# Optimization experiments

Hardware: AMD Instinct MI355X
Metric: run time of the kernel (lower is better)

## Reference

```python
import jax, jax.numpy as jnp
from jax import lax
import numpy as np

K = 31      # avg_pool2d kernel_size
PAD = 15    # avg_pool2d padding
EPS = 1.0
GAMMA = 5.0


def _box_avg(x):
    # Separable 31x31 box filter, stride 1, zero padding 15,
    # count_include_pad=True (PyTorch default) -> always divide by K*K.
    s = lax.reduce_window(x, 0.0, lax.add, (1, 1, K, 1), (1, 1, 1, 1),
                          [(0, 0), (0, 0), (PAD, PAD), (0, 0)])
    s = lax.reduce_window(s, 0.0, lax.add, (1, 1, 1, K), (1, 1, 1, 1),
                          [(0, 0), (0, 0), (0, 0), (PAD, PAD)])
    return s / (K * K)


def setup_inputs() -> dict:
    key = jax.random.key(0)
    k1, k2 = jax.random.split(key)
    shape = (64, 1, 512, 512)  # [B, C, H, W]
    inp = jax.random.uniform(k1, shape, dtype=jnp.float32)
    tgt = jax.random.uniform(k2, shape, dtype=jnp.float32)
    return {"input": inp, "target": tgt}


def reference(input, target):
    weight = 1.0 + GAMMA * jnp.abs(_box_avg(target) - target)
    intersection = jnp.sum(input * target * weight)
    denom = jnp.sum(input * weight) + jnp.sum(target * weight)
    dice = (2.0 * intersection + EPS) / (denom + EPS)
    return 1.0 - dice
```

## Files before the change

### kernel.cpp

```cpp
#include <hip/hip_runtime.h>
#include <hip/hip_bf16.h>


#define BATCH 64
#define H     512
#define W     512
#define PADR  15
#define RBAND 32
#define RING  38
#define NBLK  (BATCH * (H / RBAND))

static __device__ __forceinline__ unsigned pack2(float e, float o) {
    __hip_bfloat162 h = __float22bfloat162_rn(make_float2(e, o));
    unsigned u; __builtin_memcpy(&u, &h, 4); return u;
}
static __device__ __forceinline__ float2 unpk(unsigned u) {
    return make_float2(__uint_as_float(u << 16),
                       __uint_as_float(u & 0xffff0000u));
}

__global__ __launch_bounds__(256, 4) void fused_kernel(const float* __restrict__ tgt,
                                                       const float* __restrict__ inp,
                                                       float4* __restrict__ partials) {
    const int tid  = threadIdx.x;
    const int lane = tid & 63;
    const int wv   = tid >> 6;
    const int blk  = blockIdx.x;
    const int band = blk & 15;
    const int b    = blk >> 4;
    const int R0   = band * RBAND;
    const float* timg = tgt + (size_t)b * H * W;
    const float* iimg = inp + (size_t)b * H * W;

    __shared__ __align__(16) unsigned ring[RING * 256];

    const int col0 = lane * 8;
    const int ofs  = lane * 4;

    for (int k = 0; k < 10; ++k) {
        const int r_off = wv + 4 * k;
        if (r_off < RING) {
            const int row = R0 - 15 + r_off;
            float4 v0 = make_float4(0.f, 0.f, 0.f, 0.f), v1 = v0;
            if (row >= 0) {
                v0 = *(const float4*)(timg + (size_t)row * W + col0);
                v1 = *(const float4*)(timg + (size_t)row * W + col0 + 4);
            }
            uint4 u;
            u.x = pack2(v0.x, v0.y); u.y = pack2(v0.z, v0.w);
            u.z = pack2(v1.x, v1.y); u.w = pack2(v1.z, v1.w);
            *(uint4*)&ring[((row + RING) % RING) * 256 + ofs] = u;
        }
    }
    __syncthreads();

    const float mL1 = (lane >= 1) ? 1.f : 0.f;
    const float mR1 = (lane <= 62) ? 1.f : 0.f;
    const float mL2 = (lane >= 2) ? 1.f : 0.f;
    const float mR2 = (lane <= 61) ? 1.f : 0.f;

    float vr[8];
    #pragma unroll
    for (int k = 0; k < 8; ++k) vr[k] = 0.f;
    #pragma unroll
    for (int jj = -PADR; jj <= PADR; ++jj) {
        const int rr = R0 + wv + jj;
        const uint4 c = *(const uint4*)&ring[((rr + RING) % RING) * 256 + ofs];
        const float2 e0 = unpk(c.x), e1 = unpk(c.y), e2 = unpk(c.z), e3 = unpk(c.w);
        vr[0] += e0.x; vr[1] += e0.y; vr[2] += e1.x; vr[3] += e1.y;
        vr[4] += e2.x; vr[5] += e2.y; vr[6] += e3.x; vr[7] += e3.y;
    }

    const float inv = 1.0f / 961.0f;
    float aI = 0.f, aA = 0.f, aB = 0.f;

    for (int j = 0; j < 8; ++j) {
        const int h = R0 + 4 * j + wv;

        float4 pf0 = make_float4(0.f, 0.f, 0.f, 0.f), pf1 = pf0;
        const int prow = R0 + 4 * j + 23 + wv;
        if (j < 7 && prow < H) {
            pf0 = *(const float4*)(timg + (size_t)prow * W + col0);
            pf1 = *(const float4*)(timg + (size_t)prow * W + col0 + 4);
        }
        const float4 i0 = *(const float4*)(iimg + (size_t)h * W + col0);
        const float4 i1 = *(const float4*)(iimg + (size_t)h * W + col0 + 4);

        const uint4 tc = *(const uint4*)&ring[(h % RING) * 256 + ofs];

        uint4 ua[4], us[4];
        if (j < 7) {
            #pragma unroll
            for (int q = 0; q < 4; ++q) {
                const int ar = h + 16 + q;
                ua[q] = (ar < H) ? *(const uint4*)&ring[(ar % RING) * 256 + ofs]
                                 : make_uint4(0u, 0u, 0u, 0u);
                us[q] = *(const uint4*)&ring[(((h - 15 + q) + RING) % RING) * 256 + ofs];
            }
        }

        const float p1 = vr[0];
        const float p2 = p1 + vr[1];
        const float p3 = p2 + vr[2];
        const float p4 = p3 + vr[3];
        const float p5 = p4 + vr[4];
        const float p6 = p5 + vr[5];
        const float p7 = p6 + vr[6];
        const float s  = p7 + vr[7];
        const float f1 = s - p1, f2 = s - p2, f3 = s - p3, f4 = s - p4;
        const float f5 = s - p5, f6 = s - p6, f7 = s - p7;

        const float sL1 = __shfl_up(s, 1, 64);
        const float sR1 = __shfl_down(s, 1, 64);
        const float g1 = __shfl_up(f1, 2, 64);
        const float g2 = __shfl_up(f2, 2, 64);
        const float g3 = __shfl_up(f3, 2, 64);
        const float g4 = __shfl_up(f4, 2, 64);
        const float g5 = __shfl_up(f5, 2, 64);
        const float g6 = __shfl_up(f6, 2, 64);
        const float g7 = __shfl_up(f7, 2, 64);
        const float q1 = __shfl_down(p1, 2, 64);
        const float q2 = __shfl_down(p2, 2, 64);
        const float q3 = __shfl_down(p3, 2, 64);
        const float q4 = __shfl_down(p4, 2, 64);
        const float q5 = __shfl_down(p5, 2, 64);
        const float q6 = __shfl_down(p6, 2, 64);
        const float q7 = __shfl_down(p7, 2, 64);

        const float S3 = fmaf(mL1, sL1, fmaf(mR1, sR1, s));
        float win[8];
        win[0] = fmaf(mL2, g1, S3);
        win[1] = fmaf(mL2, g2, fmaf(mR2, q1, S3));
        win[2] = fmaf(mL2, g3, fmaf(mR2, q2, S3));
        win[3] = fmaf(mL2, g4, fmaf(mR2, q3, S3));
        win[4] = fmaf(mL2, g5, fmaf(mR2, q4, S3));
        win[5] = fmaf(mL2, g6, fmaf(mR2, q5, S3));
        win[6] = fmaf(mL2, g7, fmaf(mR2, q6, S3));
        win[7] = fmaf(mR2, q7, S3);

        const float2 t0 = unpk(tc.x), t1 = unpk(tc.y), t2 = unpk(tc.z), t3 = unpk(tc.w);
        const float tv[8] = {t0.x, t0.y, t1.x, t1.y, t2.x, t2.y, t3.x, t3.y};
        const float iv[8] = {i0.x, i0.y, i0.z, i0.w, i1.x, i1.y, i1.z, i1.w};

        #pragma unroll
        for (int k = 0; k < 8; ++k) {
            const float wgt = fmaf(5.0f, fabsf(fmaf(win[k], inv, -tv[k])), 1.0f);
            aI += iv[k] * tv[k] * wgt;
            aA += iv[k] * wgt;
            aB += tv[k] * wgt;
        }

        if (j < 7) {
            #pragma unroll
            for (int q = 0; q < 4; ++q) {
                const float2 a0 = unpk(ua[q].x), a1 = unpk(ua[q].y),
                             a2 = unpk(ua[q].z), a3 = unpk(ua[q].w);
                const float2 s0 = unpk(us[q].x), s1 = unpk(us[q].y),
                             s2 = unpk(us[q].z), s3 = unpk(us[q].w);
                vr[0] += a0.x - s0.x; vr[1] += a0.y - s0.y;
                vr[2] += a1.x - s1.x; vr[3] += a1.y - s1.y;
                vr[4] += a2.x - s2.x; vr[5] += a2.y - s2.y;
                vr[6] += a3.x - s3.x; vr[7] += a3.y - s3.y;
            }
        }
        __syncthreads();

        if (j < 7 && prow < H) {
            uint4 u;
            u.x = pack2(pf0.x, pf0.y); u.y = pack2(pf0.z, pf0.w);
            u.z = pack2(pf1.x, pf1.y); u.w = pack2(pf1.z, pf1.w);
            *(uint4*)&ring[(prow % RING) * 256 + ofs] = u;
        }
        __syncthreads();
    }

    #pragma unroll
    for (int off = 32; off > 0; off >>= 1) {
        aI += __shfl_down(aI, off, 64);
        aA += __shfl_down(aA, off, 64);
        aB += __shfl_down(aB, off, 64);
    }
    float* rf = (float*)ring;
    if (lane == 0) { rf[wv] = aI; rf[8 + wv] = aA; rf[16 + wv] = aB; }
    __syncthreads();
    if (tid == 0) {
        float4 o;
        o.x = rf[0] + rf[1] + rf[2] + rf[3];
        o.y = rf[8] + rf[9] + rf[10] + rf[11];
        o.z = rf[16] + rf[17] + rf[18] + rf[19];
        o.w = 0.f;
        partials[blk] = o;
    }
}

__global__ __launch_bounds__(1024) void reduce_kernel(const float4* __restrict__ partials,
                                                      float* __restrict__ out) {
    const int tid = threadIdx.x;
    const float4 v = partials[tid];
    float aI = v.x, aA = v.y, aB = v.z;
    #pragma unroll
    for (int off = 32; off > 0; off >>= 1) {
        aI += __shfl_down(aI, off, 64);
        aA += __shfl_down(aA, off, 64);
        aB += __shfl_down(aB, off, 64);
    }
    __shared__ float s[3][16];
    const int wvx = tid >> 6, ln = tid & 63;
    if (ln == 0) { s[0][wvx] = aI; s[1][wvx] = aA; s[2][wvx] = aB; }
    __syncthreads();
    if (tid == 0) {
        float I = 0.f, A = 0.f, Bv = 0.f;
        #pragma unroll
        for (int k = 0; k < 16; ++k) { I += s[0][k]; A += s[1][k]; Bv += s[2][k]; }
        out[0] = 1.0f - (2.0f * I + 1.0f) / (A + Bv + 1.0f);
    }
}

extern "C" void kernel_launch(void* const* d_in, const int* in_sizes, int n_in,
                              void* d_out, int out_size, void* d_ws, size_t ws_size,
                              hipStream_t stream) {
    const float* inp = (const float*)d_in[0];
    const float* tgt = (const float*)d_in[1];
    float* out = (float*)d_out;

    float4* partials = (float4*)d_ws;

    fused_kernel<<<NBLK, 256, 0, stream>>>(tgt, inp, partials);
    reduce_kernel<<<1, 1024, 0, stream>>>(partials, out);
}
```

Baseline: 150.8 us.

## Replace shared-memory bf16 ring with per-wave global-load sliding window over 8-row bands

Drops the LDS ring buffer and bf16 packing. Each wave now handles its own 8-row band independently, reading target rows directly from global memory (relying on L2/cache), and the per-iteration __syncthreads barriers go away. The trade-off is more redundant global traffic: each wave re-reads 31 halo rows to seed its vertical sum plus add/subtract rows every step, roughly 4x more target reads per output row. In exchange the computation stays in full fp32 instead of bf16.

```diff
diff --git a/kernel.cpp b/kernel.cpp
--- a/kernel.cpp
+++ b/kernel.cpp
@@ -1,23 +1,13 @@
 #include <hip/hip_runtime.h>
-#include <hip/hip_bf16.h>
 
 
 #define BATCH 64
 #define H     512
 #define W     512
-#define PADR  15
-#define RBAND 32
-#define RING  38
-#define NBLK  (BATCH * (H / RBAND))
-
-static __device__ __forceinline__ unsigned pack2(float e, float o) {
-    __hip_bfloat162 h = __float22bfloat162_rn(make_float2(e, o));
-    unsigned u; __builtin_memcpy(&u, &h, 4); return u;
-}
-static __device__ __forceinline__ float2 unpk(unsigned u) {
-    return make_float2(__uint_as_float(u << 16),
-                       __uint_as_float(u & 0xffff0000u));
-}
+#define RB    8
+#define BANDS (H / RB)
+#define TASKS (BATCH * BANDS)
+#define NBLK  (TASKS / 4)
 
 __global__ __launch_bounds__(256, 4) void fused_kernel(const float* __restrict__ tgt,
                                                        const float* __restrict__ inp,
@@ -25,34 +15,13 @@
     const int tid  = threadIdx.x;
     const int lane = tid & 63;
     const int wv   = tid >> 6;
-    const int blk  = blockIdx.x;
-    const int band = blk & 15;
-    const int b    = blk >> 4;
-    const int R0   = band * RBAND;
+    const int task = blockIdx.x * 4 + wv;
+    const int band = task & (BANDS - 1);
+    const int b    = task >> 6;
+    const int R0   = band * RB;
     const float* timg = tgt + (size_t)b * H * W;
     const float* iimg = inp + (size_t)b * H * W;
-
-    __shared__ __align__(16) unsigned ring[RING * 256];
-
     const int col0 = lane * 8;
-    const int ofs  = lane * 4;
-
-    for (int k = 0; k < 10; ++k) {
-        const int r_off = wv + 4 * k;
-        if (r_off < RING) {
-            const int row = R0 - 15 + r_off;
-            float4 v0 = make_float4(0.f, 0.f, 0.f, 0.f), v1 = v0;
-            if (row >= 0) {
-                v0 = *(const float4*)(timg + (size_t)row * W + col0);
-                v1 = *(const float4*)(timg + (size_t)row * W + col0 + 4);
-            }
-            uint4 u;
-            u.x = pack2(v0.x, v0.y); u.y = pack2(v0.z, v0.w);
-            u.z = pack2(v1.x, v1.y); u.w = pack2(v1.z, v1.w);
-            *(uint4*)&ring[((row + RING) % RING) * 256 + ofs] = u;
-        }
-    }
-    __syncthreads();
 
     const float mL1 = (lane >= 1) ? 1.f : 0.f;
     const float mR1 = (lane <= 62) ? 1.f : 0.f;
@@ -63,40 +32,38 @@
     #pragma unroll
     for (int k = 0; k < 8; ++k) vr[k] = 0.f;
     #pragma unroll
-    for (int jj = -PADR; jj <= PADR; ++jj) {
-        const int rr = R0 + wv + jj;
-        const uint4 c = *(const uint4*)&ring[((rr + RING) % RING) * 256 + ofs];
-        const float2 e0 = unpk(c.x), e1 = unpk(c.y), e2 = unpk(c.z), e3 = unpk(c.w);
-        vr[0] += e0.x; vr[1] += e0.y; vr[2] += e1.x; vr[3] += e1.y;
-        vr[4] += e2.x; vr[5] += e2.y; vr[6] += e3.x; vr[7] += e3.y;
+    for (int jj = -15; jj <= 15; ++jj) {
+        const int r = R0 + jj;
+        if (r >= 0 && r < H) {
+            const float4 a = *(const float4*)(timg + (size_t)r * W + col0);
+            const float4 c = *(const float4*)(timg + (size_t)r * W + col0 + 4);
+            vr[0] += a.x; vr[1] += a.y; vr[2] += a.z; vr[3] += a.w;
+            vr[4] += c.x; vr[5] += c.y; vr[6] += c.z; vr[7] += c.w;
+        }
     }
 
     const float inv = 1.0f / 961.0f;
     float aI = 0.f, aA = 0.f, aB = 0.f;
 
-    for (int j = 0; j < 8; ++j) {
-        const int h = R0 + 4 * j + wv;
+    #pragma unroll 2
+    for (int s = 0; s < RB; ++s) {
+        const int h  = R0 + s;
+        const int ar = h + 16;
+        const int sr = h - 15;
 
-        float4 pf0 = make_float4(0.f, 0.f, 0.f, 0.f), pf1 = pf0;
-        const int prow = R0 + 4 * j + 23 + wv;
-        if (j < 7 && prow < H) {
-            pf0 = *(const float4*)(timg + (size_t)prow * W + col0);
-            pf1 = *(const float4*)(timg + (size_t)prow * W + col0 + 4);
-        }
         const float4 i0 = *(const float4*)(iimg + (size_t)h * W + col0);
         const float4 i1 = *(const float4*)(iimg + (size_t)h * W + col0 + 4);
-
-        const uint4 tc = *(const uint4*)&ring[(h % RING) * 256 + ofs];
-
-        uint4 ua[4], us[4];
-        if (j < 7) {
-            #pragma unroll
-            for (int q = 0; q < 4; ++q) {
-                const int ar = h + 16 + q;
-                ua[q] = (ar < H) ? *(const uint4*)&ring[(ar % RING) * 256 + ofs]
-                                 : make_uint4(0u, 0u, 0u, 0u);
-                us[q] = *(const uint4*)&ring[(((h - 15 + q) + RING) % RING) * 256 + ofs];
-            }
+        const float4 t0 = *(const float4*)(timg + (size_t)h * W + col0);
+        const float4 t1 = *(const float4*)(timg + (size_t)h * W + col0 + 4);
+        float4 a0 = make_float4(0.f, 0.f, 0.f, 0.f), a1 = a0;
+        float4 u0 = a0, u1 = a0;
+        if (ar < H) {
+            a0 = *(const float4*)(timg + (size_t)ar * W + col0);
+            a1 = *(const float4*)(timg + (size_t)ar * W + col0 + 4);
+        }
+        if (sr >= 0) {
+            u0 = *(const float4*)(timg + (size_t)sr * W + col0);
+            u1 = *(const float4*)(timg + (size_t)sr * W + col0 + 4);
         }
 
         const float p1 = vr[0];
@@ -106,12 +73,12 @@
         const float p5 = p4 + vr[4];
         const float p6 = p5 + vr[5];
         const float p7 = p6 + vr[6];
-        const float s  = p7 + vr[7];
-        const float f1 = s - p1, f2 = s - p2, f3 = s - p3, f4 = s - p4;
-        const float f5 = s - p5, f6 = s - p6, f7 = s - p7;
+        const float sS = p7 + vr[7];
+        const float f1 = sS - p1, f2 = sS - p2, f3 = sS - p3, f4 = sS - p4;
+        const float f5 = sS - p5, f6 = sS - p6, f7 = sS - p7;
 
-        const float sL1 = __shfl_up(s, 1, 64);
-        const float sR1 = __shfl_down(s, 1, 64);
+        const float sL1 = __shfl_up(sS, 1, 64);
+        const float sR1 = __shfl_down(sS, 1, 64);
         const float g1 = __shfl_up(f1, 2, 64);
         const float g2 = __shfl_up(f2, 2, 64);
         const float g3 = __shfl_up(f3, 2, 64);
@@ -127,7 +94,7 @@
         const float q6 = __shfl_down(p6, 2, 64);
         const float q7 = __shfl_down(p7, 2, 64);
 
-        const float S3 = fmaf(mL1, sL1, fmaf(mR1, sR1, s));
+        const float S3 = fmaf(mL1, sL1, fmaf(mR1, sR1, sS));
         float win[8];
         win[0] = fmaf(mL2, g1, S3);
         win[1] = fmaf(mL2, g2, fmaf(mR2, q1, S3));
@@ -138,8 +105,7 @@
         win[6] = fmaf(mL2, g7, fmaf(mR2, q6, S3));
         win[7] = fmaf(mR2, q7, S3);
 
-        const float2 t0 = unpk(tc.x), t1 = unpk(tc.y), t2 = unpk(tc.z), t3 = unpk(tc.w);
-        const float tv[8] = {t0.x, t0.y, t1.x, t1.y, t2.x, t2.y, t3.x, t3.y};
+        const float tv[8] = {t0.x, t0.y, t0.z, t0.w, t1.x, t1.y, t1.z, t1.w};
         const float iv[8] = {i0.x, i0.y, i0.z, i0.w, i1.x, i1.y, i1.z, i1.w};
 
         #pragma unroll
@@ -150,28 +116,10 @@
             aB += tv[k] * wgt;
         }
 
-        if (j < 7) {
-            #pragma unroll
-            for (int q = 0; q < 4; ++q) {
-                const float2 a0 = unpk(ua[q].x), a1 = unpk(ua[q].y),
-                             a2 = unpk(ua[q].z), a3 = unpk(ua[q].w);
-                const float2 s0 = unpk(us[q].x), s1 = unpk(us[q].y),
-                             s2 = unpk(us[q].z), s3 = unpk(us[q].w);
-                vr[0] += a0.x - s0.x; vr[1] += a0.y - s0.y;
-                vr[2] += a1.x - s1.x; vr[3] += a1.y - s1.y;
-                vr[4] += a2.x - s2.x; vr[5] += a2.y - s2.y;
-                vr[6] += a3.x - s3.x; vr[7] += a3.y - s3.y;
-            }
-        }
-        __syncthreads();
-
-        if (j < 7 && prow < H) {
-            uint4 u;
-            u.x = pack2(pf0.x, pf0.y); u.y = pack2(pf0.z, pf0.w);
-            u.z = pack2(pf1.x, pf1.y); u.w = pack2(pf1.z, pf1.w);
-            *(uint4*)&ring[(prow % RING) * 256 + ofs] = u;
-        }
-        __syncthreads();
+        vr[0] += a0.x - u0.x; vr[1] += a0.y - u0.y;
+        vr[2] += a0.z - u0.z; vr[3] += a0.w - u0.w;
+        vr[4] += a1.x - u1.x; vr[5] += a1.y - u1.y;
+        vr[6] += a1.z - u1.z; vr[7] += a1.w - u1.w;
     }
 
     #pragma unroll
@@ -180,16 +128,16 @@
         aA += __shfl_down(aA, off, 64);
         aB += __shfl_down(aB, off, 64);
     }
-    float* rf = (float*)ring;
-    if (lane == 0) { rf[wv] = aI; rf[8 + wv] = aA; rf[16 + wv] = aB; }
+    __shared__ float sm[12];
+    if (lane == 0) { sm[wv] = aI; sm[4 + wv] = aA; sm[8 + wv] = aB; }
     __syncthreads();
     if (tid == 0) {
         float4 o;
-        o.x = rf[0] + rf[1] + rf[2] + rf[3];
-        o.y = rf[8] + rf[9] + rf[10] + rf[11];
-        o.z = rf[16] + rf[17] + rf[18] + rf[19];
+        o.x = sm[0] + sm[1] + sm[2] + sm[3];
+        o.y = sm[4] + sm[5] + sm[6] + sm[7];
+        o.z = sm[8] + sm[9] + sm[10] + sm[11];
         o.w = 0.f;
-        partials[blk] = o;
+        partials[blockIdx.x] = o;
     }
 }
 
```

Measured after the change: 184.8 us. 1.23x slower.

## Prefetch target and input rows one iteration ahead with incremental ring indexing

Applied to the files above, without the earlier changes.

Global loads of the next target row and the input row are issued one loop iteration ahead, so their latency overlaps a full iteration of compute. Modulo-38 ring indexing is replaced with an incrementally advanced slot index and conditional subtraction. The __syncthreads calls become raw s_barrier with sched_barrier fences and an explicit lgkmcnt wait, which removes the vmcnt drain a full sync would force. This costs more live registers under a 4-waves-per-SIMD launch bound and relies on hand-placed waitcnt for LDS ordering.

```diff
diff --git a/kernel.cpp b/kernel.cpp
--- a/kernel.cpp
+++ b/kernel.cpp
@@ -17,6 +17,9 @@
 static __device__ __forceinline__ float2 unpk(unsigned u) {
     return make_float2(__uint_as_float(u << 16),
                        __uint_as_float(u & 0xffff0000u));
+}
+static __device__ __forceinline__ int wrap38(int s) {
+    return (s >= RING) ? s - RING : s;
 }
 
 __global__ __launch_bounds__(256, 4) void fused_kernel(const float* __restrict__ tgt,
@@ -62,40 +65,54 @@
     float vr[8];
     #pragma unroll
     for (int k = 0; k < 8; ++k) vr[k] = 0.f;
-    #pragma unroll
-    for (int jj = -PADR; jj <= PADR; ++jj) {
-        const int rr = R0 + wv + jj;
-        const uint4 c = *(const uint4*)&ring[((rr + RING) % RING) * 256 + ofs];
-        const float2 e0 = unpk(c.x), e1 = unpk(c.y), e2 = unpk(c.z), e3 = unpk(c.w);
-        vr[0] += e0.x; vr[1] += e0.y; vr[2] += e1.x; vr[3] += e1.y;
-        vr[4] += e2.x; vr[5] += e2.y; vr[6] += e3.x; vr[7] += e3.y;
+    {
+        int sl = (R0 + wv + 23) % RING;
+        for (int jj = 0; jj < 31; ++jj) {
+            const uint4 c = *(const uint4*)&ring[sl * 256 + ofs];
+            const float2 e0 = unpk(c.x), e1 = unpk(c.y), e2 = unpk(c.z), e3 = unpk(c.w);
+            vr[0] += e0.x; vr[1] += e0.y; vr[2] += e1.x; vr[3] += e1.y;
+            vr[4] += e2.x; vr[5] += e2.y; vr[6] += e3.x; vr[7] += e3.y;
+            sl = wrap38(sl + 1);
+        }
     }
 
     const float inv = 1.0f / 961.0f;
     float aI = 0.f, aA = 0.f, aB = 0.f;
 
+    const int prow0 = R0 + 23 + wv;
+    float4 pc0 = *(const float4*)(timg + (size_t)prow0 * W + col0);
+    float4 pc1 = *(const float4*)(timg + (size_t)prow0 * W + col0 + 4);
+    float4 ic0 = *(const float4*)(iimg + (size_t)(R0 + wv) * W + col0);
+    float4 ic1 = *(const float4*)(iimg + (size_t)(R0 + wv) * W + col0 + 4);
+
+    int sl_h = (R0 + wv) % RING;
+
     for (int j = 0; j < 8; ++j) {
         const int h = R0 + 4 * j + wv;
 
-        float4 pf0 = make_float4(0.f, 0.f, 0.f, 0.f), pf1 = pf0;
-        const int prow = R0 + 4 * j + 23 + wv;
-        if (j < 7 && prow < H) {
-            pf0 = *(const float4*)(timg + (size_t)prow * W + col0);
-            pf1 = *(const float4*)(timg + (size_t)prow * W + col0 + 4);
-        }
-        const float4 i0 = *(const float4*)(iimg + (size_t)h * W + col0);
-        const float4 i1 = *(const float4*)(iimg + (size_t)h * W + col0 + 4);
-
-        const uint4 tc = *(const uint4*)&ring[(h % RING) * 256 + ofs];
-
+        float4 pn0 = make_float4(0.f, 0.f, 0.f, 0.f), pn1 = pn0;
+        float4 in0 = pn0, in1 = pn0;
+        const int prow_n = h + 27;
+        if (j < 6 && prow_n < H) {
+            pn0 = *(const float4*)(timg + (size_t)prow_n * W + col0);
+            pn1 = *(const float4*)(timg + (size_t)prow_n * W + col0 + 4);
+        }
+        if (j < 7) {
+            in0 = *(const float4*)(iimg + (size_t)(h + 4) * W + col0);
+            in1 = *(const float4*)(iimg + (size_t)(h + 4) * W + col0 + 4);
+        }
+
+        const uint4 tc = *(const uint4*)&ring[sl_h * 256 + ofs];
         uint4 ua[4], us[4];
         if (j < 7) {
             #pragma unroll
             for (int q = 0; q < 4; ++q) {
                 const int ar = h + 16 + q;
-                ua[q] = (ar < H) ? *(const uint4*)&ring[(ar % RING) * 256 + ofs]
+                const int sa = wrap38(sl_h + 16 + q);
+                ua[q] = (ar < H) ? *(const uint4*)&ring[sa * 256 + ofs]
                                  : make_uint4(0u, 0u, 0u, 0u);
-                us[q] = *(const uint4*)&ring[(((h - 15 + q) + RING) % RING) * 256 + ofs];
+                const int ss = wrap38(sl_h + 23 + q);
+                us[q] = *(const uint4*)&ring[ss * 256 + ofs];
             }
         }
 
@@ -140,7 +157,7 @@
 
         const float2 t0 = unpk(tc.x), t1 = unpk(tc.y), t2 = unpk(tc.z), t3 = unpk(tc.w);
         const float tv[8] = {t0.x, t0.y, t1.x, t1.y, t2.x, t2.y, t3.x, t3.y};
-        const float iv[8] = {i0.x, i0.y, i0.z, i0.w, i1.x, i1.y, i1.z, i1.w};
+        const float iv[8] = {ic0.x, ic0.y, ic0.z, ic0.w, ic1.x, ic1.y, ic1.z, ic1.w};
 
         #pragma unroll
         for (int k = 0; k < 8; ++k) {
@@ -163,15 +180,24 @@
                 vr[6] += a3.x - s3.x; vr[7] += a3.y - s3.y;
             }
         }
-        __syncthreads();
-
-        if (j < 7 && prow < H) {
+
+        __builtin_amdgcn_sched_barrier(0);
+        __builtin_amdgcn_s_barrier();
+        __builtin_amdgcn_sched_barrier(0);
+
+        if (j < 7 && (h + 23) < H) {
             uint4 u;
-            u.x = pack2(pf0.x, pf0.y); u.y = pack2(pf0.z, pf0.w);
-            u.z = pack2(pf1.x, pf1.y); u.w = pack2(pf1.z, pf1.w);
-            *(uint4*)&ring[(prow % RING) * 256 + ofs] = u;
-        }
-        __syncthreads();
+            u.x = pack2(pc0.x, pc0.y); u.y = pack2(pc0.z, pc0.w);
+            u.z = pack2(pc1.x, pc1.y); u.w = pack2(pc1.z, pc1.w);
+            *(uint4*)&ring[wrap38(sl_h + 23) * 256 + ofs] = u;
+        }
+        asm volatile("s_waitcnt lgkmcnt(0)" ::: "memory");
+        __builtin_amdgcn_sched_barrier(0);
+        __builtin_amdgcn_s_barrier();
+        __builtin_amdgcn_sched_barrier(0);
+
+        pc0 = pn0; pc1 = pn1; ic0 = in0; ic1 = in1;
+        sl_h = wrap38(sl_h + 4);
     }
 
     #pragma unroll
```

Result: no change. 149.8 us (-0.6%).

## Stage full band halo in LDS and give each wave contiguous rows without syncs

Applied to the files above, without the earlier changes.

The whole 63-row target band (32 rows plus 31 halo rows) is loaded into LDS up front, replacing the 38-row rolling ring that was refilled with prefetched rows and two block barriers per step. Each wave now handles 8 consecutive rows and slides its vertical window by one row per step, so it does one add/subtract per step instead of four. Block indices are also swizzled across batches, and launch bounds drop to 2 blocks per CU because the larger LDS buffer limits occupancy. The trade is more LDS per block and fewer resident blocks in exchange for removing the in-loop synchronisation and the redundant window updates.

```diff
diff --git a/kernel.cpp b/kernel.cpp
--- a/kernel.cpp
+++ b/kernel.cpp
@@ -5,9 +5,8 @@
 #define BATCH 64
 #define H     512
 #define W     512
-#define PADR  15
 #define RBAND 32
-#define RING  38
+#define RING  63
 #define NBLK  (BATCH * (H / RBAND))
 
 static __device__ __forceinline__ unsigned pack2(float e, float o) {
@@ -19,13 +18,14 @@
                        __uint_as_float(u & 0xffff0000u));
 }
 
-__global__ __launch_bounds__(256, 4) void fused_kernel(const float* __restrict__ tgt,
+__global__ __launch_bounds__(256, 2) void fused_kernel(const float* __restrict__ tgt,
                                                        const float* __restrict__ inp,
                                                        float4* __restrict__ partials) {
     const int tid  = threadIdx.x;
     const int lane = tid & 63;
     const int wv   = tid >> 6;
-    const int blk  = blockIdx.x;
+    const int g    = blockIdx.x;
+    const int blk  = ((g & 7) << 7) | (g >> 3);
     const int band = blk & 15;
     const int b    = blk >> 4;
     const int R0   = band * RBAND;
@@ -37,19 +37,20 @@
     const int col0 = lane * 8;
     const int ofs  = lane * 4;
 
-    for (int k = 0; k < 10; ++k) {
-        const int r_off = wv + 4 * k;
-        if (r_off < RING) {
-            const int row = R0 - 15 + r_off;
+    #pragma unroll
+    for (int k = 0; k < 16; ++k) {
+        const int idx = 4 * k + wv;
+        if (idx < RING) {
+            const int row = R0 - 15 + idx;
             float4 v0 = make_float4(0.f, 0.f, 0.f, 0.f), v1 = v0;
-            if (row >= 0) {
+            if (row >= 0 && row < H) {
                 v0 = *(const float4*)(timg + (size_t)row * W + col0);
                 v1 = *(const float4*)(timg + (size_t)row * W + col0 + 4);
             }
             uint4 u;
             u.x = pack2(v0.x, v0.y); u.y = pack2(v0.z, v0.w);
             u.z = pack2(v1.x, v1.y); u.w = pack2(v1.z, v1.w);
-            *(uint4*)&ring[((row + RING) % RING) * 256 + ofs] = u;
+            *(uint4*)&ring[idx * 256 + ofs] = u;
         }
     }
     __syncthreads();
@@ -59,13 +60,13 @@
     const float mL2 = (lane >= 2) ? 1.f : 0.f;
     const float mR2 = (lane <= 61) ? 1.f : 0.f;
 
+    const int base = 8 * wv;
     float vr[8];
     #pragma unroll
     for (int k = 0; k < 8; ++k) vr[k] = 0.f;
     #pragma unroll
-    for (int jj = -PADR; jj <= PADR; ++jj) {
-        const int rr = R0 + wv + jj;
-        const uint4 c = *(const uint4*)&ring[((rr + RING) % RING) * 256 + ofs];
+    for (int jj = 0; jj < 31; ++jj) {
+        const uint4 c = *(const uint4*)&ring[(base + jj) * 256 + ofs];
         const float2 e0 = unpk(c.x), e1 = unpk(c.y), e2 = unpk(c.z), e3 = unpk(c.w);
         vr[0] += e0.x; vr[1] += e0.y; vr[2] += e1.x; vr[3] += e1.y;
         vr[4] += e2.x; vr[5] += e2.y; vr[6] += e3.x; vr[7] += e3.y;
@@ -74,29 +75,18 @@
     const float inv = 1.0f / 961.0f;
     float aI = 0.f, aA = 0.f, aB = 0.f;
 
-    for (int j = 0; j < 8; ++j) {
-        const int h = R0 + 4 * j + wv;
-
-        float4 pf0 = make_float4(0.f, 0.f, 0.f, 0.f), pf1 = pf0;
-        const int prow = R0 + 4 * j + 23 + wv;
-        if (j < 7 && prow < H) {
-            pf0 = *(const float4*)(timg + (size_t)prow * W + col0);
-            pf1 = *(const float4*)(timg + (size_t)prow * W + col0 + 4);
-        }
+    #pragma unroll
+    for (int st = 0; st < 8; ++st) {
+        const int h  = R0 + 8 * wv + st;
+        const int sl = base + st;
+
         const float4 i0 = *(const float4*)(iimg + (size_t)h * W + col0);
         const float4 i1 = *(const float4*)(iimg + (size_t)h * W + col0 + 4);
-
-        const uint4 tc = *(const uint4*)&ring[(h % RING) * 256 + ofs];
-
-        uint4 ua[4], us[4];
-        if (j < 7) {
-            #pragma unroll
-            for (int q = 0; q < 4; ++q) {
-                const int ar = h + 16 + q;
-                ua[q] = (ar < H) ? *(const uint4*)&ring[(ar % RING) * 256 + ofs]
-                                 : make_uint4(0u, 0u, 0u, 0u);
-                us[q] = *(const uint4*)&ring[(((h - 15 + q) + RING) % RING) * 256 + ofs];
-            }
+        const uint4  tc = *(const uint4*)&ring[(sl + 15) * 256 + ofs];
+        uint4 ua = make_uint4(0u, 0u, 0u, 0u), us = ua;
+        if (st < 7) {
+            ua = *(const uint4*)&ring[(sl + 31) * 256 + ofs];
+            us = *(const uint4*)&ring[sl * 256 + ofs];
         }
 
         const float p1 = vr[0];
@@ -150,28 +140,16 @@
             aB += tv[k] * wgt;
         }
 
-        if (j < 7) {
-            #pragma unroll
-            for (int q = 0; q < 4; ++q) {
-                const float2 a0 = unpk(ua[q].x), a1 = unpk(ua[q].y),
-                             a2 = unpk(ua[q].z), a3 = unpk(ua[q].w);
-                const float2 s0 = unpk(us[q].x), s1 = unpk(us[q].y),
-                             s2 = unpk(us[q].z), s3 = unpk(us[q].w);
-                vr[0] += a0.x - s0.x; vr[1] += a0.y - s0.y;
-                vr[2] += a1.x - s1.x; vr[3] += a1.y - s1.y;
-                vr[4] += a2.x - s2.x; vr[5] += a2.y - s2.y;
-                vr[6] += a3.x - s3.x; vr[7] += a3.y - s3.y;
-            }
-        }
-        __syncthreads();
-
-        if (j < 7 && prow < H) {
-            uint4 u;
-            u.x = pack2(pf0.x, pf0.y); u.y = pack2(pf0.z, pf0.w);
-            u.z = pack2(pf1.x, pf1.y); u.w = pack2(pf1.z, pf1.w);
-            *(uint4*)&ring[(prow % RING) * 256 + ofs] = u;
-        }
-        __syncthreads();
+        if (st < 7) {
+            const float2 a0 = unpk(ua.x), a1 = unpk(ua.y),
+                         a2 = unpk(ua.z), a3 = unpk(ua.w);
+            const float2 s0 = unpk(us.x), s1 = unpk(us.y),
+                         s2 = unpk(us.z), s3 = unpk(us.w);
+            vr[0] += a0.x - s0.x; vr[1] += a0.y - s0.y;
+            vr[2] += a1.x - s1.x; vr[3] += a1.y - s1.y;
+            vr[4] += a2.x - s2.x; vr[5] += a2.y - s2.y;
+            vr[6] += a3.x - s3.x; vr[7] += a3.y - s3.y;
+        }
     }
 
     #pragma unroll
@@ -180,6 +158,7 @@
         aA += __shfl_down(aA, off, 64);
         aB += __shfl_down(aB, off, 64);
     }
+    __syncthreads();
     float* rf = (float*)ring;
     if (lane == 0) { rf[wv] = aI; rf[8 + wv] = aA; rf[16 + wv] = aB; }
     __syncthreads();
@@ -189,7 +168,7 @@
         o.y = rf[8] + rf[9] + rf[10] + rf[11];
         o.z = rf[16] + rf[17] + rf[18] + rf[19];
         o.w = 0.f;
-        partials[blk] = o;
+        partials[g] = o;
     }
 }
 
```

Measured after the change: 153.7 us. Within noise of the previous version (+1.9%).
